# Performance work log

Hardware: AMD Instinct MI355X
Metric: run time of the kernel (lower is better)

## Reference

```python
import jax, jax.numpy as jnp
import numpy as np

RMAX, SMAX, CZ = 32, 2, 128
R_BINS = 2 * RMAX + 1   # 65
S_BINS = 2 * SMAX + 1   # 5
IN_FEAT = 2 * R_BINS + S_BINS + 1  # 136
B, N = 1, 1024


def setup_inputs() -> dict:
    key = jax.random.key(0)
    ks = jax.random.split(key, 6)
    asym_id = jax.random.randint(ks[0], (B, N), 0, 8, dtype=jnp.int32)
    residue_idx = jnp.sort(jax.random.randint(ks[1], (B, N), 0, 1024, dtype=jnp.int32), axis=-1)
    entity_id = jax.random.randint(ks[2], (B, N), 0, 4, dtype=jnp.int32)
    token_idx = jnp.sort(jax.random.randint(ks[3], (B, N), 0, 1024, dtype=jnp.int32), axis=-1)
    sym_id = jax.random.randint(ks[4], (B, N), 0, 4, dtype=jnp.int32)
    # nn.Linear(136, cz, bias=False); W stored here as [in_feat, cz] (= torch weight.T)
    W = jax.random.normal(ks[5], (IN_FEAT, CZ), dtype=jnp.float32) * (1.0 / np.sqrt(IN_FEAT))
    return dict(asym_id=asym_id, residue_idx=residue_idx, entity_id=entity_id,
                token_idx=token_idx, sym_id=sym_id, W=W)


def reference(asym_id, residue_idx, entity_id, token_idx, sym_id, W):
    # pairwise equality masks, orientation matches torch unsqueeze(1)/unsqueeze(2)
    same_chain = asym_id[:, None, :] == asym_id[:, :, None]          # [B,N,N]
    same_residue = residue_idx[:, None, :] == residue_idx[:, :, None]
    same_entity = entity_id[:, None, :] == entity_id[:, :, None]

    two_rmax = jnp.int32(2 * RMAX)
    two_smax = jnp.int32(2 * SMAX)

    # torch.where(same_chain == False, clip(diff + rmax, 0, 2rmax), 2rmax)
    d_res_raw = residue_idx[:, None, :] - residue_idx[:, :, None] + RMAX
    d_residue = jnp.where(~same_chain, jnp.clip(d_res_raw, 0, two_rmax), two_rmax)

    d_tok_raw = token_idx[:, None, :] - token_idx[:, :, None] + RMAX
    d_tokens = jnp.where(jnp.logical_and(~same_residue, ~same_chain),
                         jnp.clip(d_tok_raw, 0, two_rmax), two_rmax)

    d_ch_raw = sym_id[:, None, :] - sym_id[:, :, None] + SMAX
    d_chain = jnp.where(~same_chain, jnp.clip(d_ch_raw, 0, two_smax), two_smax)

    # one_hot + concat + Linear(no bias) == gather-and-sum of the weight rows.
    # concat layout: [rel_pos (R_BINS) | rel_token (R_BINS) | same_entity (1) | rel_chain (S_BINS)]
    p = (jnp.take(W, d_residue, axis=0)
         + jnp.take(W, R_BINS + d_tokens, axis=0)
         + same_entity[..., None].astype(W.dtype) * W[2 * R_BINS]
         + jnp.take(W, 2 * R_BINS + 1 + d_chain, axis=0))   # [B,N,N,CZ]
    return p
```

## Files before the change

kernel.cpp:

```cpp
#include <hip/hip_runtime.h>


typedef float f4 __attribute__((ext_vector_type(4)));

constexpr int ROWS = 136;
constexpr int THREADS = 1024;
constexpr int GRID = 512;

__global__ __launch_bounds__(THREADS)
void relpos_kernel(const int* __restrict__ asym,
                   const int* __restrict__ resid,
                   const int* __restrict__ ent,
                   const int* __restrict__ tok,
                   const int* __restrict__ sym,
                   const float* __restrict__ W,
                   f4* __restrict__ outv)
{
    __shared__ f4 sW[ROWS * 32];
    __shared__ uint32_t sPk[1024 + 16];
    const int tid = threadIdx.x;

    const f4* Wv = reinterpret_cast<const f4*>(W);
    for (int k = tid; k < ROWS * 32; k += THREADS)
        sW[k] = Wv[k];
    {
        const uint32_t pk = (uint32_t)asym[tid]
                          | ((uint32_t)resid[tid] << 3)
                          | ((uint32_t)ent[tid]   << 13)
                          | ((uint32_t)tok[tid]   << 15)
                          | ((uint32_t)sym[tid]   << 25);
        sPk[tid] = pk;
        if (tid < 16) sPk[1024 + tid] = 0u;
    }
    __syncthreads();

    const int t  = blockIdx.x * THREADS + tid;
    const int c4 = t & 31;
    const int p0 = t >> 5;
    const int j  = p0 & 1023;
    int i        = p0 >> 10;

    const uint32_t pkj = sPk[j];
    const int aj  = pkj & 7;
    const int rj  = (pkj >> 3)  & 1023;
    const int ej  = (pkj >> 13) & 3;
    const int tj  = (pkj >> 15) & 1023;
    const int sj  = (pkj >> 25) & 3;
    const int rjb = rj + 32, tjb = tj + 32, sjb = sj + 2;

    const f4 vE = sW[130 * 32 + c4];

    size_t oidx = (size_t)t;
    uint32_t pk = sPk[i];
    #pragma unroll 4
    for (int it = 0; it < 64; ++it) {
        const uint32_t pkc = (uint32_t)__builtin_amdgcn_readfirstlane((int)pk);
        pk = sPk[i + 16];

        const int ai = pkc & 7;
        const int ri = (pkc >> 3)  & 1023;
        const int ei = (pkc >> 13) & 3;
        const int ti = (pkc >> 15) & 1023;
        const int si = (pkc >> 25) & 3;

        const bool sc  = (ai == aj);
        const bool scr = sc || (ri == rj);

        int dres = min(max(rjb - ri, 0), 64);
        int dtok = min(max(tjb - ti, 0), 64);
        int dch  = min(max(sjb - si, 0), 4);
        if (sc)  { dres = 64; dch = 4; }
        if (scr) { dtok = 64; }
        const float se = (ei == ej) ? 1.0f : 0.0f;

        const f4 v0 = sW[dres * 32 + c4];
        const f4 v1 = sW[(65 + dtok) * 32 + c4];
        const f4 v3 = sW[(131 + dch) * 32 + c4];

        f4 r;
        r.x = fmaf(se, vE.x, v0.x + v1.x) + v3.x;
        r.y = fmaf(se, vE.y, v0.y + v1.y) + v3.y;
        r.z = fmaf(se, vE.z, v0.z + v1.z) + v3.z;
        r.w = fmaf(se, vE.w, v0.w + v1.w) + v3.w;

        __builtin_nontemporal_store(r, &outv[oidx]);
        oidx += (size_t)GRID * THREADS;
        i += 16;
    }
}

extern "C" void kernel_launch(void* const* d_in, const int* in_sizes, int n_in,
                              void* d_out, int out_size, void* d_ws, size_t ws_size,
                              hipStream_t stream) {
    const int*   asym  = (const int*)  d_in[0];
    const int*   resid = (const int*)  d_in[1];
    const int*   ent   = (const int*)  d_in[2];
    const int*   tok   = (const int*)  d_in[3];
    const int*   sym   = (const int*)  d_in[4];
    const float* W     = (const float*)d_in[5];
    f4* outv = (f4*)d_out;

    relpos_kernel<<<GRID, THREADS, 0, stream>>>(asym, resid, ent, tok, sym, W, outv);
}
```

Measured before the change: 118.7 us.

## Batch eight row computations before stores and halve block size

Each thread now computes eight output vectors into registers before issuing their stores back to back. It also replaces nontemporal stores with normal stores and changes the launch to 1024 blocks of 512 threads, with the packed index table loaded in a strided loop. The aim is more memory-level parallelism on the output writes and better occupancy. The cost is more register pressure, and the output writes may now pollute the cache.

New measurement: 117.4 us. Within noise of the previous version (-1.1%).

```diff
diff --git a/kernel.cpp b/kernel.cpp
--- a/kernel.cpp
+++ b/kernel.cpp
@@ -4,8 +4,9 @@
 typedef float f4 __attribute__((ext_vector_type(4)));
 
 constexpr int ROWS = 136;
-constexpr int THREADS = 1024;
-constexpr int GRID = 512;
+constexpr int THREADS = 512;
+constexpr int GRID = 1024;
+constexpr int BATCH = 8;
 
 __global__ __launch_bounds__(THREADS)
 void relpos_kernel(const int* __restrict__ asym,
@@ -17,20 +18,18 @@
                    f4* __restrict__ outv)
 {
     __shared__ f4 sW[ROWS * 32];
-    __shared__ uint32_t sPk[1024 + 16];
+    __shared__ uint32_t sPk[1024];
     const int tid = threadIdx.x;
 
     const f4* Wv = reinterpret_cast<const f4*>(W);
     for (int k = tid; k < ROWS * 32; k += THREADS)
         sW[k] = Wv[k];
-    {
-        const uint32_t pk = (uint32_t)asym[tid]
-                          | ((uint32_t)resid[tid] << 3)
-                          | ((uint32_t)ent[tid]   << 13)
-                          | ((uint32_t)tok[tid]   << 15)
-                          | ((uint32_t)sym[tid]   << 25);
-        sPk[tid] = pk;
-        if (tid < 16) sPk[1024 + tid] = 0u;
+    for (int k = tid; k < 1024; k += THREADS) {
+        sPk[k] = (uint32_t)asym[k]
+               | ((uint32_t)resid[k] << 3)
+               | ((uint32_t)ent[k]   << 13)
+               | ((uint32_t)tok[k]   << 15)
+               | ((uint32_t)sym[k]   << 25);
     }
     __syncthreads();
 
@@ -38,54 +37,57 @@
     const int c4 = t & 31;
     const int p0 = t >> 5;
     const int j  = p0 & 1023;
-    int i        = p0 >> 10;
+    const int i0 = p0 >> 10;
 
     const uint32_t pkj = sPk[j];
     const int aj  = pkj & 7;
-    const int rj  = (pkj >> 3)  & 1023;
+    const int rjb = ((pkj >> 3)  & 1023) + 32;
     const int ej  = (pkj >> 13) & 3;
-    const int tj  = (pkj >> 15) & 1023;
-    const int sj  = (pkj >> 25) & 3;
-    const int rjb = rj + 32, tjb = tj + 32, sjb = sj + 2;
+    const int tjb = ((pkj >> 15) & 1023) + 32;
+    const int sjb = ((pkj >> 25) & 3) + 2;
+    const int rj  = rjb - 32;
 
     const f4 vE = sW[130 * 32 + c4];
 
     size_t oidx = (size_t)t;
-    uint32_t pk = sPk[i];
-    #pragma unroll 4
-    for (int it = 0; it < 64; ++it) {
-        const uint32_t pkc = (uint32_t)__builtin_amdgcn_readfirstlane((int)pk);
-        pk = sPk[i + 16];
+    for (int b8 = 0; b8 < 64 / BATCH; ++b8) {
+        f4 r[BATCH];
+        #pragma unroll
+        for (int u = 0; u < BATCH; ++u) {
+            const int i = i0 + 16 * (b8 * BATCH + u);
+            const uint32_t pkc =
+                (uint32_t)__builtin_amdgcn_readfirstlane((int)sPk[i]);
 
-        const int ai = pkc & 7;
-        const int ri = (pkc >> 3)  & 1023;
-        const int ei = (pkc >> 13) & 3;
-        const int ti = (pkc >> 15) & 1023;
-        const int si = (pkc >> 25) & 3;
+            const int ai = pkc & 7;
+            const int ri = (pkc >> 3)  & 1023;
+            const int ei = (pkc >> 13) & 3;
+            const int ti = (pkc >> 15) & 1023;
+            const int si = (pkc >> 25) & 3;
 
-        const bool sc  = (ai == aj);
-        const bool scr = sc || (ri == rj);
+            const bool sc  = (ai == aj);
+            const bool scr = sc || (ri == rj);
 
-        int dres = min(max(rjb - ri, 0), 64);
-        int dtok = min(max(tjb - ti, 0), 64);
-        int dch  = min(max(sjb - si, 0), 4);
-        if (sc)  { dres = 64; dch = 4; }
-        if (scr) { dtok = 64; }
-        const float se = (ei == ej) ? 1.0f : 0.0f;
+            int dres = min(max(rjb - ri, 0), 64);
+            int dtok = min(max(tjb - ti, 0), 64);
+            int dch  = min(max(sjb - si, 0), 4);
+            if (sc)  { dres = 64; dch = 4; }
+            if (scr) { dtok = 64; }
+            const float se = (ei == ej) ? 1.0f : 0.0f;
 
-        const f4 v0 = sW[dres * 32 + c4];
-        const f4 v1 = sW[(65 + dtok) * 32 + c4];
-        const f4 v3 = sW[(131 + dch) * 32 + c4];
+            const f4 v0 = sW[dres * 32 + c4];
+            const f4 v1 = sW[(65 + dtok) * 32 + c4];
+            const f4 v3 = sW[(131 + dch) * 32 + c4];
 
-        f4 r;
-        r.x = fmaf(se, vE.x, v0.x + v1.x) + v3.x;
-        r.y = fmaf(se, vE.y, v0.y + v1.y) + v3.y;
-        r.z = fmaf(se, vE.z, v0.z + v1.z) + v3.z;
-        r.w = fmaf(se, vE.w, v0.w + v1.w) + v3.w;
-
-        __builtin_nontemporal_store(r, &outv[oidx]);
-        oidx += (size_t)GRID * THREADS;
-        i += 16;
+            r[u].x = fmaf(se, vE.x, v0.x + v1.x) + v3.x;
+            r[u].y = fmaf(se, vE.y, v0.y + v1.y) + v3.y;
+            r[u].z = fmaf(se, vE.z, v0.z + v1.z) + v3.z;
+            r[u].w = fmaf(se, vE.w, v0.w + v1.w) + v3.w;
+        }
+        #pragma unroll
+        for (int u = 0; u < BATCH; ++u) {
+            outv[oidx] = r[u];
+            oidx += (size_t)GRID * THREADS;
+        }
     }
 }
 
```
